# Optimization experiments

Measured on AMD Instinct MI355X. Metric: run time of the kernel, lower is better.

## Reference

```python
import jax, jax.numpy as jnp
import numpy as np

BASE_SIGMAS = (2.0, 4.0, 8.0, 16.0, 32.0)
REF_LEN = 512
TRUNCATE = 4.0
STAT_WIN = 16
TEMP = 0.7
EPS = 1e-6


def _gauss_kernels(T):
    """Centered normalized Gaussian kernels, sigmas scaled by T/REF_LEN (numpy, static)."""
    s = T / REF_LEN
    ks = []
    for b in BASE_SIGMAS:
        sig = round(b * s, 4)
        R = min(max(1, int(TRUNCATE * sig + 0.5)), max(1, (T - 1) // 2))
        n = np.arange(-R, R + 1, dtype=np.float32)
        k = np.exp(-0.5 * (n / max(sig, 1e-6)) ** 2)
        ks.append((k / (k.sum() + 1e-12)).astype(np.float32))
    return ks


def _corr1d(x_pad, k):
    """Depthwise cross-correlation along time. x_pad:[B,Tp,C], k:[K] -> [B,Tp-K+1,C].
    Same kernel for every channel: fold C into batch."""
    B, Tp, C = x_pad.shape
    K = k.shape[0]
    xc = jnp.moveaxis(x_pad, 1, 2).reshape(B * C, 1, Tp)
    kern = jnp.asarray(k, x_pad.dtype).reshape(1, 1, K)
    y = jax.lax.conv_general_dilated(xc, kern, (1,), 'VALID')  # [B*C,1,Tout]
    Tout = Tp - K + 1
    return jnp.moveaxis(y.reshape(B, C, Tout), 1, 2)


def _pad_reflect_t(x, lp, rp):
    return jnp.pad(x, ((0, 0), (lp, rp), (0, 0)), mode='reflect')


def reference(x, W1, b1, W2, b2, W3, b3):
    B, T, C = x.shape
    # 1) multi-scale depthwise Gaussian smoothing -> Y [B,T,C,K]
    Ys = []
    for k in _gauss_kernels(T):
        pad = k.shape[0] // 2
        Ys.append(_corr1d(_pad_reflect_t(x, pad, pad), k))
    Y = jnp.stack(Ys, axis=-1)

    # 2) windowed local statistics via correlation kernels (== torch unfold + reduce)
    win = max(2, min(STAT_WIN, T))
    lp, rp = (win - 1) // 2, win // 2
    xp = _pad_reflect_t(x, lp, rp)
    mean_k = np.full((win,), 1.0 / win, dtype=np.float32)
    t = np.arange(win, dtype=np.float32)
    t_c = t - t.mean()
    t_var = float((t_c ** 2).sum())
    mean = _corr1d(xp, mean_k)                           # [B,T,C]
    ex2 = _corr1d(xp * xp, mean_k)
    var = jnp.maximum(ex2 - mean * mean, 0.0)
    cov = _corr1d(xp, t_c)                               # sum(x * t_centered) over window
    slope = cov / (t_var + EPS)

    std = jnp.sqrt(var + EPS)
    z = jnp.clip((x - mean) / std, -10.0, 10.0)
    log_var = jnp.log(var + EPS) / 10.0
    norm_slope = jnp.clip(slope / (std + EPS), -10.0, 10.0)
    feats = jnp.stack([z, log_var, norm_slope], axis=-1)  # [B,T,C,3]

    # 3) conditioning MLP (Linear/GELU/Linear/GELU/Linear), exact-erf GELU like torch
    h = jax.nn.gelu(jnp.einsum('btcf,hf->btch', feats, W1) + b1, approximate=False)
    h = jax.nn.gelu(jnp.einsum('btch,gh->btcg', h, W2) + b2, approximate=False)
    logits = jnp.einsum('btcg,kg->btck', h, W3) + b3      # [B,T,C,K]
    w = jax.nn.softmax(logits / TEMP, axis=-1)

    # 4) gated combine
    return (Y * w).sum(axis=-1)


def setup_inputs() -> dict:
    key = jax.random.key(0)
    ks = jax.random.split(key, 7)
    B, T, C, H, K = 32, 2048, 64, 32, 5
    return {
        'x': jax.random.normal(ks[0], (B, T, C), dtype=jnp.float32),
        'W1': jax.random.normal(ks[1], (H, 3), dtype=jnp.float32) * 0.3,
        'b1': jax.random.normal(ks[2], (H,), dtype=jnp.float32) * 0.1,
        'W2': jax.random.normal(ks[3], (H, H), dtype=jnp.float32) * 0.15,
        'b2': jax.random.normal(ks[4], (H,), dtype=jnp.float32) * 0.1,
        'W3': jax.random.normal(ks[5], (K, H), dtype=jnp.float32) * 0.05,
        'b3': jnp.zeros((K,), dtype=jnp.float32),
    }
```

## Files before the change

### kernel.cpp

```cpp
#include <hip/hip_runtime.h>
#include <hip/hip_fp16.h>
#include <math.h>

#define TT 2048
#define CC 64
#define BB 32
#define PAD 512
#define ROWL 3136

typedef __attribute__((ext_vector_type(8))) short short8;
typedef __attribute__((ext_vector_type(4))) float float4v;
typedef _Float16 half8 __attribute__((ext_vector_type(8)));

#define NSTEPS 67
__device__ unsigned short g_afrag_hi[NSTEPS * 64 * 8];

__device__ __forceinline__ float fast_rcp(float x) { return __builtin_amdgcn_rcpf(x); }
__device__ __forceinline__ float fast_exp2(float x) { return __builtin_amdgcn_exp2f(x); }
__device__ __forceinline__ float fast_log2(float x) { return __builtin_amdgcn_logf(x); }

__device__ __forceinline__ unsigned short f2bf(float x) {
  union { float f; unsigned u; } v; v.f = x;
  unsigned r = (v.u + 0x7FFFu + ((v.u >> 16) & 1u)) >> 16;
  return (unsigned short)r;
}
__device__ __forceinline__ float bf2f(unsigned short u) {
  union { unsigned u32; float f; } v; v.u32 = ((unsigned)u) << 16; return v.f;
}

__device__ __forceinline__ __half2 gelu_h2(__half2 x) {
  const __half2 c1 = __float2half2_rn(-0.10294217f);
  const __half2 c0 = __float2half2_rn(-2.3020231f);
  const __half2 one = __float2half2_rn(1.0f);
  __half2 u = __hmul2(x, x);
  __half2 w = __hmul2(x, __hfma2(c1, u, c0));
  __half2 e = h2exp2(w);
  return __hmul2(x, h2rcp(__hadd2(e, one)));
}

__global__ void init_frag() {
  __shared__ float ktap[2016];
  __shared__ double ssum[5];
  const int   Rr[5]  = {32, 64, 128, 256, 512};
  const float sg[5]  = {8.f, 16.f, 32.f, 64.f, 128.f};
  const int   off[5] = {0, 72, 208, 472, 984};
  const int tid = threadIdx.x;

  for (int idx = tid; idx < 2016; idx += 256) {
    int s = (idx < 72) ? 0 : (idx < 208) ? 1 : (idx < 472) ? 2 : (idx < 984) ? 3 : 4;
    int d = idx - off[s];
    float v = 0.f;
    if (d <= 2 * Rr[s]) {
      float n = (float)(d - Rr[s]) / sg[s];
      v = __expf(-0.5f * n * n);
    }
    ktap[idx] = v;
  }
  __syncthreads();
  if (tid < 5) {
    double sum = 0.0;
    for (int d = 0; d <= 2 * Rr[tid]; ++d) sum += (double)ktap[off[tid] + d];
    ssum[tid] = 1.0 / (sum + 1e-12);
  }
  __syncthreads();
  for (int idx = tid; idx < 2016; idx += 256) {
    int s = (idx < 72) ? 0 : (idx < 208) ? 1 : (idx < 472) ? 2 : (idx < 984) ? 3 : 4;
    ktap[idx] *= (float)ssum[s];
  }
  __syncthreads();

  const int cum[5] = {0, 3, 8, 17, 34};
  for (int e = blockIdx.x * 256 + tid; e < NSTEPS * 64; e += gridDim.x * 256) {
    int stg = e >> 6, lane = e & 63;
    int s = (stg < 3) ? 0 : (stg < 8) ? 1 : (stg < 17) ? 2 : (stg < 34) ? 3 : 4;
    int st = stg - cum[s];
    int i = lane & 15, h = lane >> 4;
    for (int e2 = 0; e2 < 8; ++e2) {
      int d = st * 32 + 8 * h + e2 - i;
      float v = (d >= 0 && d <= 2 * Rr[s]) ? ktap[off[s] + d] : 0.f;
      g_afrag_hi[e * 8 + e2] = f2bf(v);
    }
  }
}

__global__ void transpose_in(const float* __restrict__ x, unsigned short* __restrict__ xT) {
  __shared__ float tile[64][65];
  const int tid = threadIdx.x;
  const int b = blockIdx.x >> 5;
  const int t0 = (blockIdx.x & 31) * 64;

  const float* src = x + ((size_t)b * TT + t0) * CC;
  #pragma unroll
  for (int k = 0; k < 16; ++k) {
    int idx = k * 256 + tid;
    int row = idx >> 6, col = idx & 63;
    tile[row][col] = src[(size_t)row * CC + col];
  }
  __syncthreads();
  unsigned short* dst = xT + (size_t)b * CC * TT + t0;
  #pragma unroll
  for (int k = 0; k < 16; ++k) {
    int idx = k * 256 + tid;
    int c = idx >> 6, tt = idx & 63;
    dst[(size_t)c * TT + tt] = f2bf(tile[tt][c]);
  }
}

__global__ void transpose_out(const float* __restrict__ outT, float* __restrict__ out) {
  __shared__ float tile[64][65];
  const int tid = threadIdx.x;
  const int b = blockIdx.x >> 5;
  const int t0 = (blockIdx.x & 31) * 64;

  const float* src = outT + (size_t)b * CC * TT + t0;
  #pragma unroll
  for (int k = 0; k < 16; ++k) {
    int idx = k * 256 + tid;
    int cc2 = idx >> 6, tt = idx & 63;
    tile[cc2][tt] = src[(size_t)cc2 * TT + tt];
  }
  __syncthreads();
  float* dst = out + ((size_t)b * TT + t0) * CC;
  #pragma unroll
  for (int k = 0; k < 16; ++k) {
    int idx = k * 256 + tid;
    int tt = idx >> 6, cc2 = idx & 63;
    dst[(size_t)tt * CC + cc2] = tile[cc2][tt];
  }
}

template <int WSPATH>
__launch_bounds__(256, 3)
__global__ void fused_main_t(const float* __restrict__ x, const unsigned short* __restrict__ xT,
                             const float* __restrict__ W1, const float* __restrict__ b1,
                             const float* __restrict__ W2, const float* __restrict__ b2,
                             const float* __restrict__ W3, const float* __restrict__ b3,
                             float* __restrict__ outT, float* __restrict__ out) {
  __shared__ unsigned short row_hi[ROWL];
  __shared__ __half gbuf[8][5][16][18];

  const int tid = threadIdx.x;
  const int blk = blockIdx.x;
  const int c = blk & (CC - 1);
  const int b = blk >> 6;

  if (WSPATH) {
    const unsigned short* xtr = xT + (size_t)(b * CC + c) * TT;
    for (int i2 = tid; i2 < ROWL; i2 += 256) {
      int t = i2 - PAD;
      t = (t < 0) ? -t : t;
      t = (t >= TT) ? (2 * TT - 2 - t) : t;
      row_hi[i2] = xtr[t];
    }
  } else {
    const float* xrow = x + (size_t)b * TT * CC + c;
    for (int i2 = tid; i2 < ROWL; i2 += 256) {
      int t = i2 - PAD;
      t = (t < 0) ? -t : t;
      t = (t >= TT) ? (2 * TT - 2 - t) : t;
      row_hi[i2] = f2bf(xrow[(size_t)t * CC]);
    }
  }
  __syncthreads();

  const int t0 = tid * 8;
  const int lane = tid & 63;
  const int wvi = tid >> 6;

  {
    float w24[24];
    {
      const unsigned short* ph = &row_hi[PAD + t0 - 8];
      unsigned hw[12];
      *(uint4*)&hw[0] = *(const uint4*)ph;
      *(uint4*)&hw[4] = *(const uint4*)(ph + 8);
      *(uint4*)&hw[8] = *(const uint4*)(ph + 16);
      #pragma unroll
      for (int m2 = 0; m2 < 12; ++m2) {
        union { unsigned u; float f; } a, bb;
        a.u  = (hw[m2] & 0xFFFFu) << 16;
        bb.u = hw[m2] & 0xFFFF0000u;
        w24[2 * m2]     = a.f;
        w24[2 * m2 + 1] = bb.f;
      }
    }

    float sm = 0.f, sq = 0.f, scv = 0.f;
    #pragma unroll
    for (int j = 0; j < 16; ++j) {
      float v = w24[1 + j];
      sm += v;
      sq  = fmaf(v, v, sq);
      scv = fmaf(v, (float)j - 7.5f, scv);
    }

    #pragma unroll
    for (int i = 0; i < 8; ++i) {
      const float xv   = w24[i + 8];
      const float mean = sm * 0.0625f;
      const float ex2  = sq * 0.0625f;
      const float var  = fmaxf(ex2 - mean * mean, 0.f);
      const float slope = scv * (1.0f / 340.0f);
      const float stdv = sqrtf(var + 1e-6f);
      float z = (xv - mean) * fast_rcp(stdv);
      z = fminf(fmaxf(z, -10.f), 10.f);
      float lv = fast_log2(var + 1e-6f) * 0.069314718f;
      float ns = slope * fast_rcp(stdv + 1e-6f);
      ns = fminf(fmaxf(ns, -10.f), 10.f);

      const int e = t0 + i;
      const int ch = e >> 8, rr = e & 15, pp = (e >> 4) & 15;
      gbuf[ch][0][rr][pp] = __float2half(z);
      gbuf[ch][1][rr][pp] = __float2half(lv);
      gbuf[ch][2][rr][pp] = __float2half(ns);

      if (i < 7) {
        const float xo = w24[i + 1], xn = w24[i + 17];
        scv = fmaf(8.5f, xo, fmaf(7.5f, xn, scv - sm));
        sm += (xn - xo);
        sq = fmaf(xn, xn, sq);
        sq = fmaf(-xo, xo, sq);
      }
    }
  }

  {
    const int kg = lane >> 4;
    const int m  = lane & 15;
    const int ch0 = 2 * wvi, ch1 = 2 * wvi + 1;

    half8 w2f0, w2f1;
    {
      const float* p0 = W2 + (size_t)m * 32 + 8 * kg;
      const float* p1 = W2 + (size_t)(16 + m) * 32 + 8 * kg;
      #pragma unroll
      for (int e2 = 0; e2 < 8; ++e2) {
        w2f0[e2] = (_Float16)p0[e2];
        w2f1[e2] = (_Float16)p1[e2];
      }
    }

    __half2 w1z[4], w1l[4], w1n[4], b1p[4];
    #pragma unroll
    for (int p = 0; p < 4; ++p) {
      int n0 = 8 * kg + 2 * p;
      w1z[p] = __halves2half2(__float2half(W1[n0 * 3 + 0]), __float2half(W1[n0 * 3 + 3]));
      w1l[p] = __halves2half2(__float2half(W1[n0 * 3 + 1]), __float2half(W1[n0 * 3 + 4]));
      w1n[p] = __halves2half2(__float2half(W1[n0 * 3 + 2]), __float2half(W1[n0 * 3 + 5]));
      b1p[p] = __halves2half2(__float2half(b1[n0]), __float2half(b1[n0 + 1]));
    }
    float4v b2a = *(const float4v*)(b2 + 4 * kg);
    float4v b2b = *(const float4v*)(b2 + 16 + 4 * kg);
    __half2 w3p[5][4];
    #pragma unroll
    for (int k = 0; k < 5; ++k) {
      int g0 = 4 * kg;
      w3p[k][0] = __halves2half2(__float2half(W3[k * 32 + g0]),      __float2half(W3[k * 32 + g0 + 1]));
      w3p[k][1] = __halves2half2(__float2half(W3[k * 32 + g0 + 2]),  __float2half(W3[k * 32 + g0 + 3]));
      w3p[k][2] = __halves2half2(__float2half(W3[k * 32 + 16 + g0]), __float2half(W3[k * 32 + 16 + g0 + 1]));
      w3p[k][3] = __halves2half2(__float2half(W3[k * 32 + 16 + g0 + 2]), __float2half(W3[k * 32 + 16 + g0 + 3]));
    }
    const float b30 = b3[0], b31 = b3[1], b32 = b3[2], b33 = b3[3], b34 = b3[4];
    const float kS = 2.0609929f;

    auto do_col = [&](int ch, int pp) {
      __half2 z2 = __half2half2(gbuf[ch][0][m][pp]);
      __half2 l2 = __half2half2(gbuf[ch][1][m][pp]);
      __half2 n2 = __half2half2(gbuf[ch][2][m][pp]);

      union { __half2 h2[4]; half8 h8; } bu;
      #pragma unroll
      for (int p = 0; p < 4; ++p) {
        __half2 pre = __hfma2(w1z[p], z2, b1p[p]);
        pre = __hfma2(w1l[p], l2, pre);
        pre = __hfma2(w1n[p], n2, pre);
        bu.h2[p] = gelu_h2(pre);
      }

      float4v acc0 = {0.f,0.f,0.f,0.f}, acc1 = {0.f,0.f,0.f,0.f};
      acc0 = __builtin_amdgcn_mfma_f32_16x16x32_f16(w2f0, bu.h8, acc0, 0, 0, 0);
      acc1 = __builtin_amdgcn_mfma_f32_16x16x32_f16(w2f1, bu.h8, acc1, 0, 0, 0);

      __half2 hh0 = __floats2half2_rn(acc0[0] + b2a[0], acc0[1] + b2a[1]);
      __half2 hh1 = __floats2half2_rn(acc0[2] + b2a[2], acc0[3] + b2a[3]);
      __half2 hh2 = __floats2half2_rn(acc1[0] + b2b[0], acc1[1] + b2b[1]);
      __half2 hh3 = __floats2half2_rn(acc1[2] + b2b[2], acc1[3] + b2b[3]);
      hh0 = gelu_h2(hh0); hh1 = gelu_h2(hh1); hh2 = gelu_h2(hh2); hh3 = gelu_h2(hh3);

      float lg[5];
      #pragma unroll
      for (int k = 0; k < 5; ++k) {
        __half2 a = __hmul2(w3p[k][0], hh0);
        a = __hfma2(w3p[k][1], hh1, a);
        a = __hfma2(w3p[k][2], hh2, a);
        a = __hfma2(w3p[k][3], hh3, a);
        lg[k] = __low2float(a) + __high2float(a);
      }
      #pragma unroll
      for (int k = 0; k < 5; ++k) {
        lg[k] += __shfl_xor(lg[k], 16);
        lg[k] += __shfl_xor(lg[k], 32);
      }
      lg[0] += b30; lg[1] += b31; lg[2] += b32; lg[3] += b33; lg[4] += b34;

      float e0 = fast_exp2(lg[0] * kS);
      float e1 = fast_exp2(lg[1] * kS);
      float e2 = fast_exp2(lg[2] * kS);
      float e3 = fast_exp2(lg[3] * kS);
      float e4 = fast_exp2(lg[4] * kS);
      const float rs = fast_rcp(e0 + e1 + e2 + e3 + e4);

      float gw = e0;
      gw = (kg == 1) ? e1 : gw;
      gw = (kg == 2) ? e2 : gw;
      gw = (kg == 3) ? e3 : gw;
      gbuf[ch][kg][m][pp] = __float2half(gw * rs);
      if (kg == 0) gbuf[ch][4][m][pp] = __float2half(e4 * rs);
    };

    #pragma unroll 1
    for (int pp = 0; pp < 16; ++pp) {
      do_col(ch0, pp);
      do_col(ch1, pp);
    }
  }

  {
    const int hq = lane >> 4, p = lane & 15;
    const int ch0 = 2 * wvi, ch1 = 2 * wvi + 1;

    const int Rs[5]    = {32, 64, 128, 256, 512};
    const int steps[5] = {3, 5, 9, 17, 33};
    const int cum[5]   = {0, 3, 8, 17, 34};

    float4v o0 = {0.f,0.f,0.f,0.f}, o1 = {0.f,0.f,0.f,0.f};

    #pragma unroll 1
    for (int s = 0; s < 5; ++s) {
      float4v a0 = {0.f,0.f,0.f,0.f}, a1 = {0.f,0.f,0.f,0.f};
      const int eb0 = PAD + 256 * ch0 - Rs[s] + 16 * p + 8 * hq;
      const int eb1 = eb0 + 256;
      const unsigned short* ahb = g_afrag_hi + (size_t)cum[s] * 512 + lane * 8;

      for (int st = 0; st < steps[s]; ++st) {
        short8 kh = *(const short8*)(ahb + st * 512);
        short8 b0h = *(const short8*)(&row_hi[eb0 + st * 32]);
        short8 b1h = *(const short8*)(&row_hi[eb1 + st * 32]);
        a0 = __builtin_amdgcn_mfma_f32_16x16x32_bf16(kh, b0h, a0, 0, 0, 0);
        a1 = __builtin_amdgcn_mfma_f32_16x16x32_bf16(kh, b1h, a1, 0, 0, 0);
      }
      #pragma unroll
      for (int r = 0; r < 4; ++r) {
        o0[r] = fmaf(__half2float(gbuf[ch0][s][4 * hq + r][p]), a0[r], o0[r]);
        o1[r] = fmaf(__half2float(gbuf[ch1][s][4 * hq + r][p]), a1[r], o1[r]);
      }
    }

    if (WSPATH) {
      float* orow = outT + (size_t)(b * CC + c) * TT;
      *(float4v*)(orow + 256 * ch0 + 16 * p + 4 * hq) = o0;
      *(float4v*)(orow + 256 * ch1 + 16 * p + 4 * hq) = o1;
    } else {
      const size_t obase = (size_t)b * TT * CC + c;
      #pragma unroll
      for (int r = 0; r < 4; ++r) {
        out[obase + (size_t)(256 * ch0 + 16 * p + 4 * hq + r) * CC] = o0[r];
        out[obase + (size_t)(256 * ch1 + 16 * p + 4 * hq + r) * CC] = o1[r];
      }
    }
  }
}

extern "C" void kernel_launch(void* const* d_in, const int* in_sizes, int n_in,
                              void* d_out, int out_size, void* d_ws, size_t ws_size,
                              hipStream_t stream) {
  const float* x  = (const float*)d_in[0];
  const float* W1 = (const float*)d_in[1];
  const float* b1 = (const float*)d_in[2];
  const float* W2 = (const float*)d_in[3];
  const float* b2 = (const float*)d_in[4];
  const float* W3 = (const float*)d_in[5];
  const float* b3 = (const float*)d_in[6];
  float* outp = (float*)d_out;

  hipLaunchKernelGGL(init_frag, dim3(8), dim3(256), 0, stream);

  const size_t xt_bytes  = (size_t)BB * CC * TT * sizeof(unsigned short);
  const size_t ot_bytes  = (size_t)BB * CC * TT * sizeof(float);
  if (ws_size >= xt_bytes + ot_bytes) {
    unsigned short* xT = (unsigned short*)d_ws;
    float* outT = (float*)((char*)d_ws + xt_bytes);
    hipLaunchKernelGGL(transpose_in, dim3(BB * 32), dim3(256), 0, stream, x, xT);
    hipLaunchKernelGGL(fused_main_t<1>, dim3(BB * CC), dim3(256), 0, stream,
                       x, xT, W1, b1, W2, b2, W3, b3, outT, outp);
    hipLaunchKernelGGL(transpose_out, dim3(BB * 32), dim3(256), 0, stream, outT, outp);
  } else {
    hipLaunchKernelGGL(fused_main_t<0>, dim3(BB * CC), dim3(256), 0, stream,
                       x, (const unsigned short*)nullptr, W1, b1, W2, b2, W3, b3,
                       (float*)nullptr, outp);
  }
}
```

Before: 168.2 us.

## Compute third MLP layer with MFMA and fold init_frag into transpose_in

Replaces the per-lane packed-half dot products plus cross-lane xor reductions for the 5-logit output layer with a single 16x16x32 f16 MFMA. Lane shuffles gather the hidden activations into the B operand, and further shuffles pull the logits back out. Separately, the Gaussian tap fragment table is now built by the first 8 blocks of transpose_in, which drops one kernel launch on the workspace path. The trade is several extra shuffles per column, and transpose_in now carries more shared memory for every block.

```diff
diff --git a/kernel.cpp b/kernel.cpp
--- a/kernel.cpp
+++ b/kernel.cpp
@@ -24,9 +24,7 @@
   unsigned r = (v.u + 0x7FFFu + ((v.u >> 16) & 1u)) >> 16;
   return (unsigned short)r;
 }
-__device__ __forceinline__ float bf2f(unsigned short u) {
-  union { unsigned u32; float f; } v; v.u32 = ((unsigned)u) << 16; return v.f;
-}
+__device__ __forceinline__ unsigned h2u(__half2 h) { union { __half2 h; unsigned u; } c; c.h = h; return c.u; }
 
 __device__ __forceinline__ __half2 gelu_h2(__half2 x) {
   const __half2 c1 = __float2half2_rn(-0.10294217f);
@@ -38,13 +36,11 @@
   return __hmul2(x, h2rcp(__hadd2(e, one)));
 }
 
-__global__ void init_frag() {
-  __shared__ float ktap[2016];
-  __shared__ double ssum[5];
+__device__ __forceinline__ void init_frag_body(int bid, int nb, int tid,
+                                               float* ktap, double* ssum) {
   const int   Rr[5]  = {32, 64, 128, 256, 512};
   const float sg[5]  = {8.f, 16.f, 32.f, 64.f, 128.f};
   const int   off[5] = {0, 72, 208, 472, 984};
-  const int tid = threadIdx.x;
 
   for (int idx = tid; idx < 2016; idx += 256) {
     int s = (idx < 72) ? 0 : (idx < 208) ? 1 : (idx < 472) ? 2 : (idx < 984) ? 3 : 4;
@@ -70,7 +66,7 @@
   __syncthreads();
 
   const int cum[5] = {0, 3, 8, 17, 34};
-  for (int e = blockIdx.x * 256 + tid; e < NSTEPS * 64; e += gridDim.x * 256) {
+  for (int e = bid * 256 + tid; e < NSTEPS * 64; e += nb * 256) {
     int stg = e >> 6, lane = e & 63;
     int s = (stg < 3) ? 0 : (stg < 8) ? 1 : (stg < 17) ? 2 : (stg < 34) ? 3 : 4;
     int st = stg - cum[s];
@@ -83,8 +79,16 @@
   }
 }
 
+__global__ void init_frag() {
+  __shared__ float ktap[2016];
+  __shared__ double ssum[5];
+  init_frag_body(blockIdx.x, gridDim.x, threadIdx.x, ktap, ssum);
+}
+
 __global__ void transpose_in(const float* __restrict__ x, unsigned short* __restrict__ xT) {
   __shared__ float tile[64][65];
+  __shared__ float ktap[2016];
+  __shared__ double ssum[5];
   const int tid = threadIdx.x;
   const int b = blockIdx.x >> 5;
   const int t0 = (blockIdx.x & 31) * 64;
@@ -104,6 +108,7 @@
     int c = idx >> 6, tt = idx & 63;
     dst[(size_t)c * TT + tt] = f2bf(tile[tt][c]);
   }
+  if (blockIdx.x < 8) init_frag_body(blockIdx.x, 8, tid, ktap, ssum);
 }
 
 __global__ void transpose_out(const float* __restrict__ outT, float* __restrict__ out) {
@@ -239,6 +244,11 @@
         w2f1[e2] = (_Float16)p1[e2];
       }
     }
+    half8 w3f;
+    #pragma unroll
+    for (int e2 = 0; e2 < 8; ++e2) {
+      w3f[e2] = (m < 5) ? (_Float16)W3[m * 32 + 8 * kg + e2] : (_Float16)0.f;
+    }
 
     __half2 w1z[4], w1l[4], w1n[4], b1p[4];
     #pragma unroll
@@ -251,17 +261,12 @@
     }
     float4v b2a = *(const float4v*)(b2 + 4 * kg);
     float4v b2b = *(const float4v*)(b2 + 16 + 4 * kg);
-    __half2 w3p[5][4];
-    #pragma unroll
-    for (int k = 0; k < 5; ++k) {
-      int g0 = 4 * kg;
-      w3p[k][0] = __halves2half2(__float2half(W3[k * 32 + g0]),      __float2half(W3[k * 32 + g0 + 1]));
-      w3p[k][1] = __halves2half2(__float2half(W3[k * 32 + g0 + 2]),  __float2half(W3[k * 32 + g0 + 3]));
-      w3p[k][2] = __halves2half2(__float2half(W3[k * 32 + 16 + g0]), __float2half(W3[k * 32 + 16 + g0 + 1]));
-      w3p[k][3] = __halves2half2(__float2half(W3[k * 32 + 16 + g0 + 2]), __float2half(W3[k * 32 + 16 + g0 + 3]));
-    }
     const float b30 = b3[0], b31 = b3[1], b32 = b3[2], b33 = b3[3], b34 = b3[4];
     const float kS = 2.0609929f;
+
+    const int srcA = (kg & 1) * 32 + m;
+    const int srcB = srcA + 16;
+    const bool hiHalf = (kg >= 2);
 
     auto do_col = [&](int ch, int pp) {
       __half2 z2 = __half2half2(gbuf[ch][0][m][pp]);
@@ -287,27 +292,34 @@
       __half2 hh3 = __floats2half2_rn(acc1[2] + b2b[2], acc1[3] + b2b[3]);
       hh0 = gelu_h2(hh0); hh1 = gelu_h2(hh1); hh2 = gelu_h2(hh2); hh3 = gelu_h2(hh3);
 
-      float lg[5];
-      #pragma unroll
-      for (int k = 0; k < 5; ++k) {
-        __half2 a = __hmul2(w3p[k][0], hh0);
-        a = __hfma2(w3p[k][1], hh1, a);
-        a = __hfma2(w3p[k][2], hh2, a);
-        a = __hfma2(w3p[k][3], hh3, a);
-        lg[k] = __low2float(a) + __high2float(a);
-      }
-      #pragma unroll
-      for (int k = 0; k < 5; ++k) {
-        lg[k] += __shfl_xor(lg[k], 16);
-        lg[k] += __shfl_xor(lg[k], 32);
-      }
-      lg[0] += b30; lg[1] += b31; lg[2] += b32; lg[3] += b33; lg[4] += b34;
-
-      float e0 = fast_exp2(lg[0] * kS);
-      float e1 = fast_exp2(lg[1] * kS);
-      float e2 = fast_exp2(lg[2] * kS);
-      float e3 = fast_exp2(lg[3] * kS);
-      float e4 = fast_exp2(lg[4] * kS);
+      unsigned XA0 = __shfl(h2u(hh0), srcA);
+      unsigned XA1 = __shfl(h2u(hh1), srcA);
+      unsigned XA2 = __shfl(h2u(hh2), srcA);
+      unsigned XA3 = __shfl(h2u(hh3), srcA);
+      unsigned XB0 = __shfl(h2u(hh0), srcB);
+      unsigned XB1 = __shfl(h2u(hh1), srcB);
+      unsigned XB2 = __shfl(h2u(hh2), srcB);
+      unsigned XB3 = __shfl(h2u(hh3), srcB);
+      union { unsigned u[4]; half8 h8; } b2f;
+      b2f.u[0] = hiHalf ? XA2 : XA0;
+      b2f.u[1] = hiHalf ? XA3 : XA1;
+      b2f.u[2] = hiHalf ? XB2 : XB0;
+      b2f.u[3] = hiHalf ? XB3 : XB1;
+
+      float4v d2 = {0.f,0.f,0.f,0.f};
+      d2 = __builtin_amdgcn_mfma_f32_16x16x32_f16(w3f, b2f.h8, d2, 0, 0, 0);
+
+      float lg0 = __shfl(d2[0], m) + b30;
+      float lg1 = __shfl(d2[1], m) + b31;
+      float lg2 = __shfl(d2[2], m) + b32;
+      float lg3 = __shfl(d2[3], m) + b33;
+      float lg4 = __shfl(d2[0], m + 16) + b34;
+
+      float e0 = fast_exp2(lg0 * kS);
+      float e1 = fast_exp2(lg1 * kS);
+      float e2 = fast_exp2(lg2 * kS);
+      float e3 = fast_exp2(lg3 * kS);
+      float e4 = fast_exp2(lg4 * kS);
       const float rs = fast_rcp(e0 + e1 + e2 + e3 + e4);
 
       float gw = e0;
@@ -383,8 +395,6 @@
   const float* b3 = (const float*)d_in[6];
   float* outp = (float*)d_out;
 
-  hipLaunchKernelGGL(init_frag, dim3(8), dim3(256), 0, stream);
-
   const size_t xt_bytes  = (size_t)BB * CC * TT * sizeof(unsigned short);
   const size_t ot_bytes  = (size_t)BB * CC * TT * sizeof(float);
   if (ws_size >= xt_bytes + ot_bytes) {
@@ -395,6 +405,7 @@
                        x, xT, W1, b1, W2, b2, W3, b3, outT, outp);
     hipLaunchKernelGGL(transpose_out, dim3(BB * 32), dim3(256), 0, stream, outT, outp);
   } else {
+    hipLaunchKernelGGL(init_frag, dim3(8), dim3(256), 0, stream);
     hipLaunchKernelGGL(fused_main_t<0>, dim3(BB * CC), dim3(256), 0, stream,
                        x, (const unsigned short*)nullptr, W1, b1, W2, b2, W3, b3,
                        (float*)nullptr, outp);
```

After: 151.1 us. 10.2% less time.
